# Optimization experiments

Measured on AMD Instinct MI355X. Metric: run time of the kernel, lower is better.

The kernel has to match this reference:

```python
import jax, jax.numpy as jnp
import numpy as np

jax.config.update("jax_enable_x64", True)

PRIME = (1 << 31) - 1  # Mersenne prime; products with <2^31 operands fit in int64
N_DIGITS = 16
N_ARY = 32
EMB = 64
NUM_EMB = 100000    # importance-weight table rows
NUM_BUCKETS = 65536  # shared bucket table rows
NUM_HASHES = 2

_rng = np.random.RandomState(42)
SEQ_A = jnp.asarray(_rng.randint(1, PRIME, size=(N_DIGITS,)), dtype=jnp.int64)   # per-position keys for prefix hash
HASH_A = jnp.asarray(_rng.randint(1, PRIME, size=(NUM_HASHES,)), dtype=jnp.int64)
HASH_B = jnp.asarray(_rng.randint(0, PRIME, size=(NUM_HASHES,)), dtype=jnp.int64)


def _prefix_hashes(seq):
    # seq: [B, D] int64 sense codes, 0 = padding (mask_zero: zeros contribute nothing)
    h = jnp.cumsum(SEQ_A[None, :] * (seq.astype(jnp.int64) % PRIME), axis=-1) % PRIME  # [B, D]
    # pad_trailing_zeroes=True: positions past the code length repeat the last valid hash
    lengths = jnp.sum(seq != 0, axis=-1, keepdims=True)               # [B, 1]
    pos = jnp.arange(seq.shape[-1], dtype=jnp.int64)[None, :]
    idx = jnp.minimum(pos, jnp.maximum(lengths - 1, 0))
    return jnp.take_along_axis(h, idx, axis=-1)                        # [B, D]


def setup_inputs() -> dict:
    key = jax.random.key(0)
    k1, k2, k3, k4 = jax.random.split(key, 4)
    B = 4096
    input_sequence = jax.random.randint(k1, (B, N_DIGITS), 0, N_ARY, dtype=jnp.int64)
    t_representation = jax.random.normal(k2, (B, N_DIGITS, EMB), dtype=jnp.float32)
    importance_weights = jax.random.normal(k3, (NUM_EMB, NUM_HASHES), dtype=jnp.float32)
    bucket_table = jax.random.normal(k4, (NUM_BUCKETS, N_ARY * EMB), dtype=jnp.float32) * 0.02
    return {
        "input_sequence": input_sequence,
        "t_representation": t_representation,
        "importance_weights": importance_weights,
        "bucket_table": bucket_table,
    }


def reference(input_sequence, t_representation, importance_weights, bucket_table):
    ids = _prefix_hashes(input_sequence)                  # [B, D] prefix hash ids
    w = importance_weights[ids % NUM_EMB]                 # [B, D, H] importance weights
    emb = jnp.zeros(ids.shape + (bucket_table.shape[-1],), dtype=bucket_table.dtype)
    for h in range(NUM_HASHES):
        bucket = ((HASH_A[h] * ids + HASH_B[h]) % PRIME) % NUM_BUCKETS
        emb = emb + w[..., h:h + 1] * bucket_table[bucket]  # [B, D, N_ARY*EMB]
    B, D = ids.shape
    t_weight = emb.reshape(B, D, N_ARY, EMB).astype(t_representation.dtype)
    # torch.matmul(t_weight, rep.unsqueeze(-1)).squeeze(-1) -> [B, D, N_ARY]
    return jnp.einsum('bdae,bde->bda', t_weight, t_representation)
```

## Files before the change

### kernel.cpp

```cpp
#include <hip/hip_runtime.h>
#include <stdint.h>

#define PRIME 2147483647LL
#define NUM_EMB 100000
#define NUM_BUCKETS 65536
#define EMB 64
#define N_ARY 32
#define NDIG 16

struct HashConsts {
  long long seqA[NDIG];
  long long hashA[2];
  long long hashB[2];
};

__global__ __launch_bounds__(256) void hash_logits_kernel(
    const int* __restrict__ seq,
    const float* __restrict__ rep,
    const float* __restrict__ iw,
    const float* __restrict__ bt,
    float* __restrict__ out,
    HashConsts hc)
{
  const int bid  = blockIdx.x;
  const int b    = bid >> 2;
  const int wave = threadIdx.x >> 6;
  const int d    = ((bid & 3) << 2) | wave;
  const int lane = threadIdx.x & 63;
  const int g    = lane >> 4;
  const int sub  = lane & 15;

  const int* srow = seq + b * NDIG;
  int v[NDIG];
  int len = 0;
#pragma unroll
  for (int j = 0; j < NDIG; ++j) { v[j] = srow[j]; len += (v[j] != 0); }
  int idx = min(d, max(len - 1, 0));
  long long acc = 0;
#pragma unroll
  for (int j = 0; j < NDIG; ++j) {
    if (j <= idx) acc += hc.seqA[j] * (long long)v[j];
  }
  const long long id = acc % PRIME;

  const int widx = (int)(id % NUM_EMB);
  const float w0 = iw[widx * 2 + 0];
  const float w1 = iw[widx * 2 + 1];
  const unsigned int bk0 =
      (unsigned int)((hc.hashA[0] * id + hc.hashB[0]) % PRIME) & (NUM_BUCKETS - 1);
  const unsigned int bk1 =
      (unsigned int)((hc.hashA[1] * id + hc.hashB[1]) % PRIME) & (NUM_BUCKETS - 1);

  const float4* row0 = (const float4*)(bt + (size_t)bk0 * (N_ARY * EMB));
  const float4* row1 = (const float4*)(bt + (size_t)bk1 * (N_ARY * EMB));
  const float4 r = *(const float4*)(rep + ((size_t)b * NDIG + d) * EMB + sub * 4);

  float s[8];
#pragma unroll
  for (int k = 0; k < 8; ++k) {
    float4 v0 = row0[lane + 64 * k];
    float4 v1 = row1[lane + 64 * k];
    float ex = w0 * v0.x + w1 * v1.x;
    float ey = w0 * v0.y + w1 * v1.y;
    float ez = w0 * v0.z + w1 * v1.z;
    float ew = w0 * v0.w + w1 * v1.w;
    s[k] = ex * r.x + ey * r.y + ez * r.z + ew * r.w;
  }
#pragma unroll
  for (int m = 1; m <= 8; m <<= 1) {
#pragma unroll
    for (int k = 0; k < 8; ++k) s[k] += __shfl_xor(s[k], m, 64);
  }
  if (sub == 0) {
    float* obase = out + ((size_t)b * NDIG + d) * N_ARY + g;
#pragma unroll
    for (int k = 0; k < 8; ++k) obase[4 * k] = s[k];
  }
}

extern "C" void kernel_launch(void* const* d_in, const int* in_sizes, int n_in,
                              void* d_out, int out_size, void* d_ws, size_t ws_size,
                              hipStream_t stream) {
  uint32_t mt[624];
  int mti;
  mt[0] = 42u;
  for (int i = 1; i < 624; ++i)
    mt[i] = 1812433253u * (mt[i - 1] ^ (mt[i - 1] >> 30)) + (uint32_t)i;
  mti = 624;
  auto next32 = [&]() -> uint32_t {
    if (mti >= 624) {
      for (int i = 0; i < 624; ++i) {
        uint32_t y = (mt[i] & 0x80000000u) | (mt[(i + 1) % 624] & 0x7fffffffu);
        uint32_t x = mt[(i + 397) % 624] ^ (y >> 1);
        if (y & 1u) x ^= 2567483615u;
        mt[i] = x;
      }
      mti = 0;
    }
    uint32_t y = mt[mti++];
    y ^= y >> 11;
    y ^= (y << 7) & 2636928640u;
    y ^= (y << 15) & 4022730752u;
    y ^= y >> 18;
    return y;
  };
  auto draw = [&](uint32_t rng_incl) -> uint32_t {
    uint32_t val;
    do { val = next32() & 0x7FFFFFFFu; } while (val > rng_incl);
    return val;
  };
  HashConsts hc;
  for (int i = 0; i < NDIG; ++i) hc.seqA[i] = 1LL + (long long)draw(2147483645u);
  for (int i = 0; i < 2; ++i)    hc.hashA[i] = 1LL + (long long)draw(2147483645u);
  for (int i = 0; i < 2; ++i)    hc.hashB[i] = (long long)draw(2147483646u);

  const int*   seq = (const int*)d_in[0];
  const float* rep = (const float*)d_in[1];
  const float* iw  = (const float*)d_in[2];
  const float* bt  = (const float*)d_in[3];
  float*       out = (float*)d_out;

  const int B = in_sizes[0] / NDIG;
  dim3 grid(B * 4), block(256);
  hipLaunchKernelGGL(hash_logits_kernel, grid, block, 0, stream,
                     seq, rep, iw, bt, out, hc);
}
```

Baseline: 720.7 us.

## Group lookups by bucket so each table row is read once

Replaces the per-(batch,digit) gather with a bucket-sorted scheme. A first pass computes hash ids, stores importance weights, and appends each (pair, hash) entry to a per-bucket slot list, sending entries past a fixed cap to an overflow list. A gather kernel then loads each bucket row once and accumulates weighted dot products into the zeroed output with atomics. The aim is to avoid re-reading popular 8KB bucket rows from memory, at the cost of four launches, global atomics, nondeterministic float summation and scattered loads of the representation rows.

```diff
diff --git a/kernel.cpp b/kernel.cpp
--- a/kernel.cpp
+++ b/kernel.cpp
@@ -7,6 +7,7 @@
 #define EMB 64
 #define N_ARY 32
 #define NDIG 16
+#define CAP 16
 
 struct HashConsts {
   long long seqA[NDIG];
@@ -14,22 +15,121 @@
   long long hashB[2];
 };
 
+__global__ __launch_bounds__(256) void zero_kernel(uint4* __restrict__ wsv, int n_ws,
+                                                   uint4* __restrict__ outv, int n_out) {
+  int i = blockIdx.x * blockDim.x + threadIdx.x;
+  int stride = gridDim.x * blockDim.x;
+  uint4 z = make_uint4(0u, 0u, 0u, 0u);
+  for (int k = i; k < n_ws; k += stride) wsv[k] = z;
+  for (int k = i; k < n_out; k += stride) outv[k] = z;
+}
+
+__global__ __launch_bounds__(256) void pass1_kernel(
+    const int* __restrict__ seq, const float* __restrict__ iw, HashConsts hc,
+    uint32_t* __restrict__ cnt, uint32_t* __restrict__ slots,
+    float2* __restrict__ wpair, int2* __restrict__ ovf, uint32_t* __restrict__ ovfcnt,
+    int npairs) {
+  int tid = blockIdx.x * 256 + threadIdx.x;
+  if (tid >= npairs) return;
+  int b = tid >> 4, d = tid & 15;
+  const int* srow = seq + b * NDIG;
+  int vj[NDIG];
+  int len = 0;
+#pragma unroll
+  for (int j = 0; j < NDIG; ++j) { vj[j] = srow[j]; len += (vj[j] != 0); }
+  int idx = min(d, max(len - 1, 0));
+  long long acc = 0;
+#pragma unroll
+  for (int j = 0; j < NDIG; ++j)
+    if (j <= idx) acc += hc.seqA[j] * (long long)vj[j];
+  long long id = acc % PRIME;
+  int widx = (int)(id % NUM_EMB);
+  wpair[tid] = make_float2(iw[widx * 2 + 0], iw[widx * 2 + 1]);
+#pragma unroll
+  for (int h = 0; h < 2; ++h) {
+    unsigned int bk =
+        (unsigned int)((hc.hashA[h] * id + hc.hashB[h]) % PRIME) & (NUM_BUCKETS - 1);
+    uint32_t slot = atomicAdd(&cnt[bk], 1u);
+    uint32_t entry = ((uint32_t)tid << 1) | (uint32_t)h;
+    if (slot < CAP) slots[bk * CAP + slot] = entry;
+    else {
+      uint32_t o = atomicAdd(ovfcnt, 1u);
+      ovf[o] = make_int2((int)entry, (int)bk);
+    }
+  }
+}
+
+__global__ __launch_bounds__(256) void gather_kernel(
+    const float* __restrict__ bt, const float* __restrict__ rep,
+    const uint32_t* __restrict__ cnt, const uint32_t* __restrict__ slots,
+    const float2* __restrict__ wpair, float* __restrict__ out) {
+  const int bkt = blockIdx.x;
+  int n = (int)cnt[bkt];
+  if (n == 0) return;
+  if (n > CAP) n = CAP;
+  const int t = threadIdx.x;
+  const float4* rowp = (const float4*)(bt + (size_t)bkt * (N_ARY * EMB));
+  float4 ra = rowp[t * 2 + 0];
+  float4 rb = rowp[t * 2 + 1];
+  const int a = t >> 3;
+  const int eg = t & 7;
+  for (int u = 0; u < n; ++u) {
+    uint32_t s = slots[bkt * CAP + u];
+    int pair = (int)(s >> 1);
+    int h = (int)(s & 1u);
+    float2 wp = wpair[pair];
+    float w = h ? wp.y : wp.x;
+    const float4* rp = (const float4*)(rep + (size_t)pair * EMB + eg * 8);
+    float4 c0 = rp[0], c1 = rp[1];
+    float p = ra.x * c0.x + ra.y * c0.y + ra.z * c0.z + ra.w * c0.w +
+              rb.x * c1.x + rb.y * c1.y + rb.z * c1.z + rb.w * c1.w;
+    p += __shfl_xor(p, 1, 64);
+    p += __shfl_xor(p, 2, 64);
+    p += __shfl_xor(p, 4, 64);
+    if (eg == 0) atomicAdd(out + (size_t)pair * N_ARY + a, w * p);
+  }
+}
+
+__global__ __launch_bounds__(256) void overflow_kernel(
+    const float* __restrict__ bt, const float* __restrict__ rep,
+    const int2* __restrict__ ovf, const uint32_t* __restrict__ ovfcnt,
+    const float2* __restrict__ wpair, float* __restrict__ out) {
+  const uint32_t n = *ovfcnt;
+  const int t = threadIdx.x;
+  const int a = t >> 3;
+  const int eg = t & 7;
+  for (uint32_t e = blockIdx.x; e < n; e += gridDim.x) {
+    int2 en = ovf[e];
+    int pair = en.x >> 1;
+    int h = en.x & 1;
+    int bkt = en.y;
+    const float4* rowp = (const float4*)(bt + (size_t)bkt * (N_ARY * EMB));
+    float4 ra = rowp[t * 2 + 0];
+    float4 rb = rowp[t * 2 + 1];
+    float2 wp = wpair[pair];
+    float w = h ? wp.y : wp.x;
+    const float4* rp = (const float4*)(rep + (size_t)pair * EMB + eg * 8);
+    float4 c0 = rp[0], c1 = rp[1];
+    float p = ra.x * c0.x + ra.y * c0.y + ra.z * c0.z + ra.w * c0.w +
+              rb.x * c1.x + rb.y * c1.y + rb.z * c1.z + rb.w * c1.w;
+    p += __shfl_xor(p, 1, 64);
+    p += __shfl_xor(p, 2, 64);
+    p += __shfl_xor(p, 4, 64);
+    if (eg == 0) atomicAdd(out + (size_t)pair * N_ARY + a, w * p);
+  }
+}
+
 __global__ __launch_bounds__(256) void hash_logits_kernel(
-    const int* __restrict__ seq,
-    const float* __restrict__ rep,
-    const float* __restrict__ iw,
-    const float* __restrict__ bt,
-    float* __restrict__ out,
-    HashConsts hc)
-{
-  const int bid  = blockIdx.x;
-  const int b    = bid >> 2;
+    const int* __restrict__ seq, const float* __restrict__ rep,
+    const float* __restrict__ iw, const float* __restrict__ bt,
+    float* __restrict__ out, HashConsts hc) {
+  const int bid = blockIdx.x;
+  const int b = bid >> 2;
   const int wave = threadIdx.x >> 6;
-  const int d    = ((bid & 3) << 2) | wave;
+  const int d = ((bid & 3) << 2) | wave;
   const int lane = threadIdx.x & 63;
-  const int g    = lane >> 4;
-  const int sub  = lane & 15;
-
+  const int g = lane >> 4;
+  const int sub = lane & 15;
   const int* srow = seq + b * NDIG;
   int v[NDIG];
   int len = 0;
@@ -38,11 +138,9 @@
   int idx = min(d, max(len - 1, 0));
   long long acc = 0;
 #pragma unroll
-  for (int j = 0; j < NDIG; ++j) {
+  for (int j = 0; j < NDIG; ++j)
     if (j <= idx) acc += hc.seqA[j] * (long long)v[j];
-  }
   const long long id = acc % PRIME;
-
   const int widx = (int)(id % NUM_EMB);
   const float w0 = iw[widx * 2 + 0];
   const float w1 = iw[widx * 2 + 1];
@@ -50,11 +148,9 @@
       (unsigned int)((hc.hashA[0] * id + hc.hashB[0]) % PRIME) & (NUM_BUCKETS - 1);
   const unsigned int bk1 =
       (unsigned int)((hc.hashA[1] * id + hc.hashB[1]) % PRIME) & (NUM_BUCKETS - 1);
-
   const float4* row0 = (const float4*)(bt + (size_t)bk0 * (N_ARY * EMB));
   const float4* row1 = (const float4*)(bt + (size_t)bk1 * (N_ARY * EMB));
   const float4 r = *(const float4*)(rep + ((size_t)b * NDIG + d) * EMB + sub * 4);
-
   float s[8];
 #pragma unroll
   for (int k = 0; k < 8; ++k) {
@@ -111,17 +207,54 @@
   };
   HashConsts hc;
   for (int i = 0; i < NDIG; ++i) hc.seqA[i] = 1LL + (long long)draw(2147483645u);
-  for (int i = 0; i < 2; ++i)    hc.hashA[i] = 1LL + (long long)draw(2147483645u);
-  for (int i = 0; i < 2; ++i)    hc.hashB[i] = (long long)draw(2147483646u);
-
-  const int*   seq = (const int*)d_in[0];
+  for (int i = 0; i < 2; ++i) hc.hashA[i] = 1LL + (long long)draw(2147483645u);
+  for (int i = 0; i < 2; ++i) hc.hashB[i] = (long long)draw(2147483646u);
+
+  const int* seq = (const int*)d_in[0];
   const float* rep = (const float*)d_in[1];
-  const float* iw  = (const float*)d_in[2];
-  const float* bt  = (const float*)d_in[3];
-  float*       out = (float*)d_out;
+  const float* iw = (const float*)d_in[2];
+  const float* bt = (const float*)d_in[3];
+  float* out = (float*)d_out;
 
   const int B = in_sizes[0] / NDIG;
-  dim3 grid(B * 4), block(256);
-  hipLaunchKernelGGL(hash_logits_kernel, grid, block, 0, stream,
-                     seq, rep, iw, bt, out, hc);
-}
+  const int npairs = B * NDIG;
+
+  const size_t off_cnt = 0;
+  const size_t sz_cnt = (size_t)NUM_BUCKETS * 4;
+  const size_t off_meta_end = sz_cnt + 16;
+  const size_t off_ovf = off_meta_end;
+  const size_t sz_ovf = (size_t)npairs * 2 * 8;
+  const size_t off_wpair = off_ovf + sz_ovf;
+  const size_t sz_wpair = (size_t)npairs * 8;
+  const size_t off_slots = off_wpair + sz_wpair;
+  const size_t sz_slots = (size_t)NUM_BUCKETS * CAP * 4;
+  const size_t need = off_slots + sz_slots;
+
+  if (ws_size < need) {
+    dim3 grid(B * 4), block(256);
+    hipLaunchKernelGGL(hash_logits_kernel, grid, block, 0, stream,
+                       seq, rep, iw, bt, out, hc);
+    return;
+  }
+
+  char* ws = (char*)d_ws;
+  uint32_t* cnt = (uint32_t*)(ws + off_cnt);
+  uint32_t* ovfcnt = (uint32_t*)(ws + sz_cnt);
+  int2* ovf = (int2*)(ws + off_ovf);
+  float2* wpair = (float2*)(ws + off_wpair);
+  uint32_t* slots = (uint32_t*)(ws + off_slots);
+
+  int n_ws_vec = (int)(off_meta_end / 16);
+  int n_out_vec = out_size / 4;
+  hipLaunchKernelGGL(zero_kernel, dim3(1024), dim3(256), 0, stream,
+                     (uint4*)ws, n_ws_vec, (uint4*)out, n_out_vec);
+
+  hipLaunchKernelGGL(pass1_kernel, dim3((npairs + 255) / 256), dim3(256), 0, stream,
+                     seq, iw, hc, cnt, slots, wpair, ovf, ovfcnt, npairs);
+
+  hipLaunchKernelGGL(gather_kernel, dim3(NUM_BUCKETS), dim3(256), 0, stream,
+                     bt, rep, cnt, slots, wpair, out);
+
+  hipLaunchKernelGGL(overflow_kernel, dim3(128), dim3(256), 0, stream,
+                     bt, rep, ovf, ovfcnt, wpair, out);
+}
```

Result: slower. 767.9 us (+6.5%).
